# Kernel tuning notes

Hardware: AMD Instinct MI355X
Metric: run time of the kernel (lower is better)

Reference implementation:

```python
import jax, jax.numpy as jnp
import numpy as np

VOCAB = 100000
NUM_INTERNAL = VOCAB - 1
EMBED = 128
BATCH = 16384
CTX = 10
MAX_CODE = 24


def setup_inputs() -> dict:
    key = jax.random.key(0)
    k1, k2, k3, k4, k5, k6 = jax.random.split(key, 6)
    context_words = jax.random.randint(k1, (BATCH, CTX), 0, VOCAB, dtype=jnp.int64 if jax.config.jax_enable_x64 else jnp.int32)
    paths = jax.random.randint(k2, (BATCH, MAX_CODE), 0, NUM_INTERNAL, dtype=jnp.int32)
    codes = jax.random.randint(k3, (BATCH, MAX_CODE), 0, 2, dtype=jnp.int32)
    mask = jax.random.randint(k4, (BATCH, MAX_CODE), 0, 2, dtype=jnp.int32).astype(bool)
    W_in = jax.random.normal(k5, (VOCAB, EMBED), dtype=jnp.float32) * 0.1
    W_internal = jax.random.normal(k6, (NUM_INTERNAL, EMBED), dtype=jnp.float32) * 0.1
    return {"context_words": context_words, "paths": paths, "codes": codes,
            "mask": mask, "W_in": W_in, "W_internal": W_internal}


def reference(context_words, paths, codes, mask, W_in, W_internal):
    # CBOW context vector: mean of input embeddings over the context window
    ctx_emb = W_in[context_words]                      # [B, C, D]
    context_vector = jnp.mean(ctx_emb, axis=1)         # [B, D]

    # Hierarchical softmax: gather internal-node embeddings along each Huffman path
    node_emb = W_internal[paths]                       # [B, L, D]
    scores = jnp.einsum('bd,bld->bl', context_vector, node_emb)  # [B, L]

    # bit==1 -> -logsigmoid(score); bit==0 -> -logsigmoid(-score)
    sign = (2 * codes - 1).astype(scores.dtype)        # [B, L] in {-1, +1}
    step_loss = -jax.nn.log_sigmoid(sign * scores)     # [B, L]
    step_loss = jnp.where(mask, step_loss, 0.0)

    total_loss = jnp.sum(step_loss) / BATCH
    return total_loss
```

## Files before the change

kernel.cpp:

```cpp
#include <hip/hip_runtime.h>

#define BATCH 16384
#define CTX 10
#define MAXC 24
#define ROWS_PER_BLOCK 8
#define GRID_MAIN (BATCH / ROWS_PER_BLOCK)

__global__ __launch_bounds__(256) void cbow_hs_main(
    const int* __restrict__ ctx_words,
    const int* __restrict__ paths,
    const int* __restrict__ codes,
    const int* __restrict__ mask,
    const float* __restrict__ W_in,
    const float* __restrict__ W_internal,
    float* __restrict__ partials)
{
    const int tid  = threadIdx.x;
    const int lane = tid & 63;
    const int half = lane >> 5;
    const int l5   = lane & 31;
    const int wave = tid >> 6;
    const int row  = blockIdx.x * ROWS_PER_BLOCK + wave * 2 + half;

    const float4* Win4 = (const float4*)W_in;
    const float4* Wn4  = (const float4*)W_internal;

    float4 acc = make_float4(0.f, 0.f, 0.f, 0.f);
#pragma unroll
    for (int k = 0; k < CTX; ++k) {
        const int w = ctx_words[row * CTX + k];
        const float4 e = Win4[(long)w * 32 + l5];
        acc.x += e.x; acc.y += e.y; acc.z += e.z; acc.w += e.w;
    }
    const float inv = 1.0f / (float)CTX;
    acc.x *= inv; acc.y *= inv; acc.z *= inv; acc.w *= inv;

    float part[MAXC];
#pragma unroll
    for (int l = 0; l < MAXC; ++l) {
        const int p = paths[row * MAXC + l];
        const float4 e = Wn4[(long)p * 32 + l5];
        part[l] = acc.x * e.x + acc.y * e.y + acc.z * e.z + acc.w * e.w;
    }

#pragma unroll
    for (int off = 16; off; off >>= 1) {
#pragma unroll
        for (int l = 0; l < MAXC; ++l)
            part[l] += __shfl_xor(part[l], off, 64);
    }

    float total = 0.f;
#pragma unroll
    for (int l = 0; l < MAXC; ++l) {
        const int c = codes[row * MAXC + l];
        const int m = mask[row * MAXC + l];
        const float s = part[l];
        const float z = c ? s : -s;
        const float loss = fmaxf(-z, 0.f) + log1pf(expf(-fabsf(z)));
        total += m ? loss : 0.f;
    }

    __shared__ float red[ROWS_PER_BLOCK];
    if (l5 == 0) red[wave * 2 + half] = total;
    __syncthreads();
    if (tid == 0) {
        float s = 0.f;
#pragma unroll
        for (int i = 0; i < ROWS_PER_BLOCK; ++i) s += red[i];
        partials[blockIdx.x] = s;
    }
}

__global__ __launch_bounds__(256) void cbow_hs_reduce(
    const float* __restrict__ partials, float* __restrict__ out)
{
    const int tid = threadIdx.x;
    float s = 0.f;
#pragma unroll
    for (int i = 0; i < GRID_MAIN / 256; ++i)
        s += partials[tid + i * 256];
#pragma unroll
    for (int off = 32; off; off >>= 1)
        s += __shfl_xor(s, off, 64);
    __shared__ float red[4];
    if ((tid & 63) == 0) red[tid >> 6] = s;
    __syncthreads();
    if (tid == 0)
        out[0] = (red[0] + red[1] + red[2] + red[3]) * (1.0f / (float)BATCH);
}

extern "C" void kernel_launch(void* const* d_in, const int* in_sizes, int n_in,
                              void* d_out, int out_size, void* d_ws, size_t ws_size,
                              hipStream_t stream) {
    const int*   ctx_words  = (const int*)d_in[0];
    const int*   paths      = (const int*)d_in[1];
    const int*   codes      = (const int*)d_in[2];
    const int*   mask       = (const int*)d_in[3];
    const float* W_in       = (const float*)d_in[4];
    const float* W_internal = (const float*)d_in[5];
    float* out      = (float*)d_out;
    float* partials = (float*)d_ws;

    cbow_hs_main<<<GRID_MAIN, 256, 0, stream>>>(
        ctx_words, paths, codes, mask, W_in, W_internal, partials);
    cbow_hs_reduce<<<1, 256, 0, stream>>>(partials, out);
}
```

Before: 165.9 us.

## Use transpose-style butterfly reduction and one-wave blocks with per-lane loss

Replaces the 24 independent 5-step shuffle reductions with a recursive-halving butterfly, so each round exchanges half as many values and every lane ends up holding one path score. The loss is then computed once per lane in parallel instead of 24 times redundantly, and reduced with a full-wave shuffle. Blocks shrink to a single 64-thread wave, which removes shared memory and __syncthreads but creates four times as many blocks and partials for the final reduce kernel to sum.

Result: slower. 186.4 us (+12.4%).

```diff
diff --git a/kernel.cpp b/kernel.cpp
--- a/kernel.cpp
+++ b/kernel.cpp
@@ -3,10 +3,9 @@
 #define BATCH 16384
 #define CTX 10
 #define MAXC 24
-#define ROWS_PER_BLOCK 8
-#define GRID_MAIN (BATCH / ROWS_PER_BLOCK)
+#define GRID_MAIN (BATCH / 2)
 
-__global__ __launch_bounds__(256) void cbow_hs_main(
+__global__ __launch_bounds__(64) void cbow_hs_main(
     const int* __restrict__ ctx_words,
     const int* __restrict__ paths,
     const int* __restrict__ codes,
@@ -15,12 +14,10 @@
     const float* __restrict__ W_internal,
     float* __restrict__ partials)
 {
-    const int tid  = threadIdx.x;
-    const int lane = tid & 63;
+    const int lane = threadIdx.x;
     const int half = lane >> 5;
     const int l5   = lane & 31;
-    const int wave = tid >> 6;
-    const int row  = blockIdx.x * ROWS_PER_BLOCK + wave * 2 + half;
+    const int row  = blockIdx.x * 2 + half;
 
     const float4* Win4 = (const float4*)W_in;
     const float4* Wn4  = (const float4*)W_internal;
@@ -35,41 +32,43 @@
     const float inv = 1.0f / (float)CTX;
     acc.x *= inv; acc.y *= inv; acc.z *= inv; acc.w *= inv;
 
-    float part[MAXC];
+    float v[32];
+#pragma unroll
+    for (int l = 0; l < 32; ++l) v[l] = 0.f;
 #pragma unroll
     for (int l = 0; l < MAXC; ++l) {
         const int p = paths[row * MAXC + l];
         const float4 e = Wn4[(long)p * 32 + l5];
-        part[l] = acc.x * e.x + acc.y * e.y + acc.z * e.z + acc.w * e.w;
+        v[l] = acc.x * e.x + acc.y * e.y + acc.z * e.z + acc.w * e.w;
     }
 
 #pragma unroll
     for (int off = 16; off; off >>= 1) {
+        const bool hi = (l5 & off) != 0;
 #pragma unroll
-        for (int l = 0; l < MAXC; ++l)
-            part[l] += __shfl_xor(part[l], off, 64);
+        for (int k = 0; k < off; ++k) {
+            const float send = hi ? v[k] : v[k + off];
+            const float recv = __shfl_xor(send, off, 64);
+            const float keep = hi ? v[k + off] : v[k];
+            v[k] = keep + recv;
+        }
+    }
+    const float score = v[0];
+
+    float loss = 0.f;
+    if (l5 < MAXC) {
+        const int c = codes[row * MAXC + l5];
+        const int m = mask[row * MAXC + l5];
+        const float z = c ? score : -score;
+        const float sp = fmaxf(-z, 0.f) + log1pf(expf(-fabsf(z)));
+        loss = m ? sp : 0.f;
     }
 
-    float total = 0.f;
 #pragma unroll
-    for (int l = 0; l < MAXC; ++l) {
-        const int c = codes[row * MAXC + l];
-        const int m = mask[row * MAXC + l];
-        const float s = part[l];
-        const float z = c ? s : -s;
-        const float loss = fmaxf(-z, 0.f) + log1pf(expf(-fabsf(z)));
-        total += m ? loss : 0.f;
-    }
-
-    __shared__ float red[ROWS_PER_BLOCK];
-    if (l5 == 0) red[wave * 2 + half] = total;
-    __syncthreads();
-    if (tid == 0) {
-        float s = 0.f;
-#pragma unroll
-        for (int i = 0; i < ROWS_PER_BLOCK; ++i) s += red[i];
-        partials[blockIdx.x] = s;
-    }
+    for (int off = 32; off; off >>= 1)
+        loss += __shfl_xor(loss, off, 64);
+    if (lane == 0)
+        partials[blockIdx.x] = loss;
 }
 
 __global__ __launch_bounds__(256) void cbow_hs_reduce(
@@ -102,7 +101,7 @@
     float* out      = (float*)d_out;
     float* partials = (float*)d_ws;
 
-    cbow_hs_main<<<GRID_MAIN, 256, 0, stream>>>(
+    cbow_hs_main<<<GRID_MAIN, 64, 0, stream>>>(
         ctx_words, paths, codes, mask, W_in, W_internal, partials);
     cbow_hs_reduce<<<1, 256, 0, stream>>>(partials, out);
 }
```
